# Optimization experiments

Hardware: AMD Instinct MI355X
Metric: run time of the kernel (lower is better)

## Reference

```python
import jax, jax.numpy as jnp
import numpy as np

N_HEADS = 16
HIDDEN = 1024
HEAD = HIDDEN // N_HEADS


def setup_inputs() -> dict:
    key = jax.random.key(0)
    ks = jax.random.split(key, 11)
    B, S, H = 2, 2048, HIDDEN
    s = 1.0 / np.sqrt(H)
    return {
        "query": jax.random.normal(ks[0], (B, S, H), jnp.float32),
        "key": jax.random.normal(ks[1], (B, S, H), jnp.float32),
        "value": jax.random.normal(ks[2], (B, S, H), jnp.float32),
        "Wq": jax.random.normal(ks[3], (H, H), jnp.float32) * s,
        "bq": jnp.zeros((H,), jnp.float32),
        "Wk": jax.random.normal(ks[4], (H, H), jnp.float32) * s,
        "bk": jnp.zeros((H,), jnp.float32),
        "Wv": jax.random.normal(ks[5], (H, H), jnp.float32) * s,
        "bv": jnp.zeros((H,), jnp.float32),
        "Wo": jax.random.normal(ks[6], (H, H), jnp.float32) * s,
        "bo": jnp.zeros((H,), jnp.float32),
    }


def reference(query, key, value, Wq, bq, Wk, bk, Wv, bv, Wo, bo):
    B, Sq, H = query.shape
    Sk = key.shape[1]
    # QKV projections, split heads: [B, n_heads, S, head]
    q = (query @ Wq + bq).reshape(B, Sq, N_HEADS, HEAD).transpose(0, 2, 1, 3)
    k = (key @ Wk + bk).reshape(B, Sk, N_HEADS, HEAD).transpose(0, 2, 1, 3)
    v = (value @ Wv + bv).reshape(B, Sk, N_HEADS, HEAD).transpose(0, 2, 1, 3)
    # scaled dot-product attention (no mask, dropout p=0)
    scores = jnp.einsum("bhqd,bhkd->bhqk", q, k) / np.sqrt(HEAD).astype(np.float32)
    attn = jax.nn.softmax(scores, axis=-1)
    out = jnp.einsum("bhqk,bhkd->bhqd", attn, v)
    out = out.transpose(0, 2, 1, 3).reshape(B, Sq, H)
    return out @ Wo + bo
```

## Files before the change

kernel.cpp:

```cpp
#include <hip/hip_runtime.h>
#include <hip/hip_bf16.h>
#include <stdint.h>

typedef unsigned short u16;
typedef short bf16x8 __attribute__((ext_vector_type(8)));
typedef float f32x4 __attribute__((ext_vector_type(4)));

#define DEVI static __device__ __forceinline__

#if __has_builtin(__builtin_amdgcn_exp2f)
#define EXP2F(x) __builtin_amdgcn_exp2f(x)
#else
#define EXP2F(x) exp2f(x)
#endif

DEVI u16 f2bf(float f) {
  union { float f; uint32_t u; } v; v.f = f;
  uint32_t u = v.u;
  u += 0x7fffu + ((u >> 16) & 1u);
  return (u16)(u >> 16);
}
DEVI uint32_t pk2bf(float lo, float hi) {
  __hip_bfloat162 h = __float22bfloat162_rn(float2{lo, hi});
  union { __hip_bfloat162 h; uint32_t u; } v; v.h = h; return v.u;
}

DEVI void async16(const void* g, const void* l) {
  __builtin_amdgcn_global_load_lds(
      (const __attribute__((address_space(1))) void*)g,
      (__attribute__((address_space(3))) void*)l, 16, 0, 0);
}

DEVI f32x4 mfma16(bf16x8 a, bf16x8 b, f32x4 c) {
  return __builtin_amdgcn_mfma_f32_16x16x32_bf16(a, b, c, 0, 0, 0);
}

#define CSC 0.18033688011112042f

__global__ void convx(const float* __restrict__ q, const float* __restrict__ k,
                      const float* __restrict__ v, u16* __restrict__ out) {
  const int z = blockIdx.y;
  const float* src = (z == 0) ? q : (z == 1) ? k : v;
  const int i = (blockIdx.x * 256 + threadIdx.x) * 4;
  float4 f = *(const float4*)(src + i);
  ushort4 o;
  o.x = f2bf(f.x); o.y = f2bf(f.y); o.z = f2bf(f.z); o.w = f2bf(f.w);
  *(ushort4*)(out + (size_t)z * 4194304 + i) = o;
}

__global__ void transw(const float* __restrict__ Wq, const float* __restrict__ Wk,
                       const float* __restrict__ Wv, const float* __restrict__ Wo,
                       u16* __restrict__ WT) {
  __shared__ u16 tile[64 * 68];
  const int z = blockIdx.z;
  const float* W = (z == 0) ? Wq : (z == 1) ? Wk : (z == 2) ? Wv : Wo;
  u16* out = WT + (size_t)z * 1048576;
  const int R0 = blockIdx.y * 64, C0 = blockIdx.x * 64;
  const int t = threadIdx.x;
#pragma unroll
  for (int it = 0; it < 16; ++it) {
    int j = it * 256 + t;
    int r = j >> 6, c = j & 63;
    tile[r * 68 + c] = f2bf(W[(size_t)(R0 + r) * 1024 + C0 + c]);
  }
  __syncthreads();
#pragma unroll
  for (int it = 0; it < 16; ++it) {
    int j = it * 256 + t;
    int c = j >> 6, r = j & 63;
    out[(size_t)(C0 + c) * 1024 + R0 + r] = tile[r * 68 + c];
  }
}

__global__ __launch_bounds__(256, 3)
void qkv_gemm(const u16* __restrict__ XB, const u16* __restrict__ WT,
              const float* __restrict__ bq, const float* __restrict__ bk,
              const float* __restrict__ bv,
              u16* __restrict__ QN, u16* __restrict__ KN, u16* __restrict__ VT) {
  __shared__ u16 smem[16896];
  u16* lA = smem;
  u16* lB = smem + 8192;
  const int z = blockIdx.y;
  const u16* A  = XB + (size_t)z * 4194304;
  const u16* Bt = WT + (size_t)z * 1048576;
  const float* bias = (z == 0) ? bq : (z == 1) ? bk : bv;
  const int T = blockIdx.x;
  const int m0 = (T & 31) * 128, n0 = (T >> 5) * 128;
  const int t = threadIdx.x, lane = t & 63, w = t >> 6;
  const int quad = lane >> 4, l16 = lane & 15;
  const int wm = (w & 1) * 64, wn = (w >> 1) * 64;

  f32x4 acc[4][4] = {};
  for (int kt = 0; kt < 16; ++kt) {
    const int k0 = kt * 64;
#pragma unroll
    for (int it = 0; it < 4; ++it) {
      int i = it * 256 + t;
      int r = i >> 3, cc = i & 7, c = cc ^ (r & 7);
      async16(A + (size_t)(m0 + r) * 1024 + k0 + c * 8, &lA[i * 8]);
      async16(Bt + (size_t)(n0 + r) * 1024 + k0 + c * 8, &lB[i * 8]);
    }
    __syncthreads();
#pragma unroll
    for (int ks = 0; ks < 2; ++ks) {
      bf16x8 af[4], bfr[4];
#pragma unroll
      for (int rt = 0; rt < 4; ++rt) {
        int row = wm + rt * 16 + l16;
        af[rt] = *(const bf16x8*)&lA[row * 64 + ((ks * 4 + quad) ^ (row & 7)) * 8];
      }
#pragma unroll
      for (int ct = 0; ct < 4; ++ct) {
        int row = wn + ct * 16 + l16;
        bfr[ct] = *(const bf16x8*)&lB[row * 64 + ((ks * 4 + quad) ^ (row & 7)) * 8];
      }
#pragma unroll
      for (int rt = 0; rt < 4; ++rt)
#pragma unroll
        for (int ct = 0; ct < 4; ++ct)
          acc[rt][ct] = mfma16(bfr[ct], af[rt], acc[rt][ct]);
    }
    __syncthreads();
  }

  if (z < 2) {
    const float scl = (z == 0) ? CSC : 1.0f;
#pragma unroll
    for (int rt = 0; rt < 4; ++rt) {
      int sl = wm + rt * 16 + l16;
#pragma unroll
      for (int ct = 0; ct < 4; ++ct) {
        int nb = wn + ct * 16 + quad * 4;
        float4 b4 = *(const float4*)&bias[n0 + nb];
        ushort4 pk;
        pk.x = f2bf((acc[rt][ct][0] + b4.x) * scl);
        pk.y = f2bf((acc[rt][ct][1] + b4.y) * scl);
        pk.z = f2bf((acc[rt][ct][2] + b4.z) * scl);
        pk.w = f2bf((acc[rt][ct][3] + b4.w) * scl);
        *(ushort4*)&smem[sl * 132 + nb] = pk;
      }
    }
    __syncthreads();
    u16* out = (z == 0) ? QN : KN;
#pragma unroll
    for (int p = 0; p < 8; ++p) {
      int idx = p * 256 + t;
      int row = idx >> 4, chunk = idx & 15;
      *(bf16x8*)&out[(size_t)(m0 + row) * 1024 + n0 + chunk * 8] =
          *(const bf16x8*)&smem[row * 132 + chunk * 8];
    }
  } else {
#pragma unroll
    for (int rt = 0; rt < 4; ++rt) {
      int sl = wm + rt * 16 + l16;
#pragma unroll
      for (int ct = 0; ct < 4; ++ct) {
        int nb = wn + ct * 16 + quad * 4;
        float4 b4 = *(const float4*)&bias[n0 + nb];
        smem[(nb + 0) * 132 + sl] = f2bf(acc[rt][ct][0] + b4.x);
        smem[(nb + 1) * 132 + sl] = f2bf(acc[rt][ct][1] + b4.y);
        smem[(nb + 2) * 132 + sl] = f2bf(acc[rt][ct][2] + b4.z);
        smem[(nb + 3) * 132 + sl] = f2bf(acc[rt][ct][3] + b4.w);
      }
    }
    __syncthreads();
    const int bb = m0 >> 11, sb = m0 & 2047;
#pragma unroll
    for (int p = 0; p < 8; ++p) {
      int idx = p * 256 + t;
      int dl = idx >> 4, chunk = idx & 15;
      int ncol = n0 + dl, hh = ncol >> 6, dd = ncol & 63;
      *(bf16x8*)&VT[((size_t)((bb * 16 + hh) * 64 + dd)) * 2048 + sb + chunk * 8] =
          *(const bf16x8*)&smem[dl * 132 + chunk * 8];
    }
  }
}

__global__ __launch_bounds__(512, 2)
void attn6(const u16* __restrict__ QN, const u16* __restrict__ KN,
           const u16* __restrict__ VT, u16* __restrict__ AO) {
  __shared__ u16 lK[2][64 * 64];
  __shared__ u16 lV[2][64 * 64];
  __shared__ u16 lPT[8][32 * 72];
  const int qt0 = blockIdx.x, h = blockIdx.y, b = blockIdx.z;
  const int t = threadIdx.x, lane = t & 63, w = t >> 6;
  const int quad = lane >> 4, l16 = lane & 15;
  const u16* Qg = QN + ((size_t)(b * 2048 + qt0 * 256)) * 1024 + h * 64;
  const u16* Kg = KN + ((size_t)b * 2048) * 1024 + h * 64;
  const u16* Vg = VT + ((size_t)((b * 16 + h) * 64)) * 2048;

  bf16x8 qf[2][2];
#pragma unroll
  for (int qs = 0; qs < 2; ++qs)
#pragma unroll
    for (int ks = 0; ks < 2; ++ks)
      qf[qs][ks] = *(const bf16x8*)(Qg + (size_t)(w * 32 + qs * 16 + l16) * 1024 +
                                    ks * 32 + quad * 8);

  {
    int r = t >> 3, cc = t & 7, c = cc ^ (r & 7);
    async16(Kg + (size_t)r * 1024 + c * 8, &lK[0][t * 8]);
    async16(Vg + (size_t)r * 2048 + c * 8, &lV[0][t * 8]);
  }
  __syncthreads();

  f32x4 o[2][4] = {};
  float lsum[2] = {0.f, 0.f};
  u16* myP = &lPT[w][0];

  for (int kt = 0; kt < 32; ++kt) {
    const int cur = kt & 1, nxt = cur ^ 1;
    if (kt + 1 < 32) {
      const int kb = (kt + 1) * 64;
      int r = t >> 3, cc = t & 7, c = cc ^ (r & 7);
      async16(Kg + (size_t)(kb + r) * 1024 + c * 8, &lK[nxt][t * 8]);
      async16(Vg + (size_t)r * 2048 + kb + c * 8, &lV[nxt][t * 8]);
    }

    f32x4 sc[2][4];
    __builtin_amdgcn_s_setprio(1);
#pragma unroll
    for (int st = 0; st < 4; ++st) {
      int row = st * 16 + l16;
      bf16x8 kf0 = *(const bf16x8*)&lK[cur][row * 64 + ((quad) ^ (row & 7)) * 8];
      bf16x8 kf1 = *(const bf16x8*)&lK[cur][row * 64 + ((4 + quad) ^ (row & 7)) * 8];
#pragma unroll
      for (int qs = 0; qs < 2; ++qs) {
        f32x4 z = {};
        sc[qs][st] = mfma16(kf0, qf[qs][0], z);
        sc[qs][st] = mfma16(kf1, qf[qs][1], sc[qs][st]);
      }
    }
    __builtin_amdgcn_s_setprio(0);

#pragma unroll
    for (int qs = 0; qs < 2; ++qs)
#pragma unroll
      for (int st = 0; st < 4; ++st) {
        float p0 = EXP2F(sc[qs][st][0]);
        float p1 = EXP2F(sc[qs][st][1]);
        float p2 = EXP2F(sc[qs][st][2]);
        float p3 = EXP2F(sc[qs][st][3]);
        lsum[qs] += (p0 + p1) + (p2 + p3);
        uint2 pk;
        pk.x = pk2bf(p0, p1);
        pk.y = pk2bf(p2, p3);
        *(uint2*)&myP[(qs * 16 + l16) * 72 + st * 16 + quad * 4] = pk;
      }

    __builtin_amdgcn_s_setprio(1);
#pragma unroll
    for (int ks2 = 0; ks2 < 2; ++ks2) {
      bf16x8 pf0 = *(const bf16x8*)&myP[(l16) * 72 + ks2 * 32 + quad * 8];
      bf16x8 pf1 = *(const bf16x8*)&myP[(16 + l16) * 72 + ks2 * 32 + quad * 8];
#pragma unroll
      for (int dt = 0; dt < 4; ++dt) {
        int row = dt * 16 + l16;
        bf16x8 vf = *(const bf16x8*)&lV[cur][row * 64 + ((ks2 * 4 + quad) ^ (row & 7)) * 8];
        o[0][dt] = mfma16(vf, pf0, o[0][dt]);
        o[1][dt] = mfma16(vf, pf1, o[1][dt]);
      }
    }
    __builtin_amdgcn_s_setprio(0);
    __syncthreads();
  }

#pragma unroll
  for (int qs = 0; qs < 2; ++qs) {
    float l = lsum[qs];
    l += __shfl_xor(l, 16, 64);
    l += __shfl_xor(l, 32, 64);
    float inv = 1.0f / l;
    int qglob = qt0 * 256 + w * 32 + qs * 16 + l16;
    size_t base = ((size_t)(b * 2048 + qglob)) * 1024 + h * 64;
#pragma unroll
    for (int dt = 0; dt < 4; ++dt) {
      ushort4 pk;
      pk.x = f2bf(o[qs][dt][0] * inv);
      pk.y = f2bf(o[qs][dt][1] * inv);
      pk.z = f2bf(o[qs][dt][2] * inv);
      pk.w = f2bf(o[qs][dt][3] * inv);
      *(ushort4*)&AO[base + dt * 16 + quad * 4] = pk;
    }
  }
}

__global__ __launch_bounds__(256, 2)
void oproj_gemm(const u16* __restrict__ AO, const u16* __restrict__ Bt,
                const float* __restrict__ bias, float* __restrict__ out) {
  __shared__ u16 lA[128 * 64];
  __shared__ u16 lB[64 * 64];
  const int T = blockIdx.x;
  const int m0 = (T & 31) * 128, n0 = (T >> 5) * 64;
  const int t = threadIdx.x, lane = t & 63, w = t >> 6;
  const int quad = lane >> 4, l16 = lane & 15;
  const int wm = (w & 1) * 64, wn = (w >> 1) * 32;

  f32x4 acc[4][2] = {};
  for (int kt = 0; kt < 16; ++kt) {
    const int k0 = kt * 64;
#pragma unroll
    for (int it = 0; it < 4; ++it) {
      int i = it * 256 + t;
      int r = i >> 3, cc = i & 7, c = cc ^ (r & 7);
      async16(AO + (size_t)(m0 + r) * 1024 + k0 + c * 8, &lA[i * 8]);
    }
#pragma unroll
    for (int it = 0; it < 2; ++it) {
      int i = it * 256 + t;
      int r = i >> 3, cc = i & 7, c = cc ^ (r & 7);
      async16(Bt + (size_t)(n0 + r) * 1024 + k0 + c * 8, &lB[i * 8]);
    }
    __syncthreads();
#pragma unroll
    for (int ks = 0; ks < 2; ++ks) {
      bf16x8 af[4], bfr[2];
#pragma unroll
      for (int rt = 0; rt < 4; ++rt) {
        int row = wm + rt * 16 + l16;
        af[rt] = *(const bf16x8*)&lA[row * 64 + ((ks * 4 + quad) ^ (row & 7)) * 8];
      }
#pragma unroll
      for (int ct = 0; ct < 2; ++ct) {
        int row = wn + ct * 16 + l16;
        bfr[ct] = *(const bf16x8*)&lB[row * 64 + ((ks * 4 + quad) ^ (row & 7)) * 8];
      }
#pragma unroll
      for (int rt = 0; rt < 4; ++rt)
#pragma unroll
        for (int ct = 0; ct < 2; ++ct)
          acc[rt][ct] = mfma16(af[rt], bfr[ct], acc[rt][ct]);
    }
    __syncthreads();
  }

#pragma unroll
  for (int ct = 0; ct < 2; ++ct) {
    int ncol = n0 + wn + ct * 16 + l16;
    float bvv = bias[ncol];
#pragma unroll
    for (int rt = 0; rt < 4; ++rt)
#pragma unroll
      for (int r = 0; r < 4; ++r) {
        int m = m0 + wm + rt * 16 + quad * 4 + r;
        out[(size_t)m * 1024 + ncol] = acc[rt][ct][r] + bvv;
      }
  }
}

extern "C" void kernel_launch(void* const* d_in, const int* in_sizes, int n_in,
                              void* d_out, int out_size, void* d_ws, size_t ws_size,
                              hipStream_t stream) {
  const float* query = (const float*)d_in[0];
  const float* key   = (const float*)d_in[1];
  const float* value = (const float*)d_in[2];
  const float* Wq = (const float*)d_in[3];
  const float* bq = (const float*)d_in[4];
  const float* Wk = (const float*)d_in[5];
  const float* bk = (const float*)d_in[6];
  const float* Wv = (const float*)d_in[7];
  const float* bv = (const float*)d_in[8];
  const float* Wo = (const float*)d_in[9];
  const float* bo = (const float*)d_in[10];
  float* out = (float*)d_out;

  u16* WT = (u16*)d_ws;
  u16* QN = WT + 4 * 1048576;
  u16* KN = QN + 4194304;
  u16* VT = KN + 4194304;
  u16* XB = VT + 4194304;
  u16* AO = XB;

  convx<<<dim3(4096, 3), 256, 0, stream>>>(query, key, value, XB);
  transw<<<dim3(16, 16, 4), 256, 0, stream>>>(Wq, Wk, Wv, Wo, WT);
  qkv_gemm<<<dim3(256, 3), 256, 0, stream>>>(XB, WT, bq, bk, bv, QN, KN, VT);
  attn6<<<dim3(8, 16, 2), 512, 0, stream>>>(QN, KN, VT, AO);
  oproj_gemm<<<dim3(512), 256, 0, stream>>>(AO, WT + 3 * 1048576, bo, out);
}
```

Before: 218.1 us.

## Halve attention block to 128 queries with 4 waves, double grid size

The attention kernel now uses 256-thread blocks covering 128 query rows instead of 512 threads covering 256. This doubles the grid to 512 blocks so the GPU's compute units fill more evenly, with a launch bound of 3 blocks per CU. Each thread now issues two async K/V tile loads. The P staging stride changes from 72 to 76, which alters the LDS bank pattern. The trade-off is that K/V tiles are reloaded twice as often across the grid, and the sync granularity per block changes.

Result: slower. 241.6 us (+10.8%).

```diff
diff --git a/kernel.cpp b/kernel.cpp
--- a/kernel.cpp
+++ b/kernel.cpp
@@ -36,6 +36,8 @@
 }
 
 #define CSC 0.18033688011112042f
+
+#define PSTR 76
 
 __global__ void convx(const float* __restrict__ q, const float* __restrict__ k,
                       const float* __restrict__ v, u16* __restrict__ out) {
@@ -176,16 +178,16 @@
   }
 }
 
-__global__ __launch_bounds__(512, 2)
-void attn6(const u16* __restrict__ QN, const u16* __restrict__ KN,
+__global__ __launch_bounds__(256, 3)
+void attn7(const u16* __restrict__ QN, const u16* __restrict__ KN,
            const u16* __restrict__ VT, u16* __restrict__ AO) {
   __shared__ u16 lK[2][64 * 64];
   __shared__ u16 lV[2][64 * 64];
-  __shared__ u16 lPT[8][32 * 72];
+  __shared__ u16 lPT[4][32 * PSTR];
   const int qt0 = blockIdx.x, h = blockIdx.y, b = blockIdx.z;
   const int t = threadIdx.x, lane = t & 63, w = t >> 6;
   const int quad = lane >> 4, l16 = lane & 15;
-  const u16* Qg = QN + ((size_t)(b * 2048 + qt0 * 256)) * 1024 + h * 64;
+  const u16* Qg = QN + ((size_t)(b * 2048 + qt0 * 128)) * 1024 + h * 64;
   const u16* Kg = KN + ((size_t)b * 2048) * 1024 + h * 64;
   const u16* Vg = VT + ((size_t)((b * 16 + h) * 64)) * 2048;
 
@@ -197,10 +199,12 @@
       qf[qs][ks] = *(const bf16x8*)(Qg + (size_t)(w * 32 + qs * 16 + l16) * 1024 +
                                     ks * 32 + quad * 8);
 
-  {
-    int r = t >> 3, cc = t & 7, c = cc ^ (r & 7);
-    async16(Kg + (size_t)r * 1024 + c * 8, &lK[0][t * 8]);
-    async16(Vg + (size_t)r * 2048 + c * 8, &lV[0][t * 8]);
+#pragma unroll
+  for (int p = 0; p < 2; ++p) {
+    int i = p * 256 + t;
+    int r = i >> 3, cc = i & 7, c = cc ^ (r & 7);
+    async16(Kg + (size_t)r * 1024 + c * 8, &lK[0][i * 8]);
+    async16(Vg + (size_t)r * 2048 + c * 8, &lV[0][i * 8]);
   }
   __syncthreads();
 
@@ -212,9 +216,13 @@
     const int cur = kt & 1, nxt = cur ^ 1;
     if (kt + 1 < 32) {
       const int kb = (kt + 1) * 64;
-      int r = t >> 3, cc = t & 7, c = cc ^ (r & 7);
-      async16(Kg + (size_t)(kb + r) * 1024 + c * 8, &lK[nxt][t * 8]);
-      async16(Vg + (size_t)r * 2048 + kb + c * 8, &lV[nxt][t * 8]);
+#pragma unroll
+      for (int p = 0; p < 2; ++p) {
+        int i = p * 256 + t;
+        int r = i >> 3, cc = i & 7, c = cc ^ (r & 7);
+        async16(Kg + (size_t)(kb + r) * 1024 + c * 8, &lK[nxt][i * 8]);
+        async16(Vg + (size_t)r * 2048 + kb + c * 8, &lV[nxt][i * 8]);
+      }
     }
 
     f32x4 sc[2][4];
@@ -245,14 +253,14 @@
         uint2 pk;
         pk.x = pk2bf(p0, p1);
         pk.y = pk2bf(p2, p3);
-        *(uint2*)&myP[(qs * 16 + l16) * 72 + st * 16 + quad * 4] = pk;
+        *(uint2*)&myP[(qs * 16 + l16) * PSTR + st * 16 + quad * 4] = pk;
       }
 
     __builtin_amdgcn_s_setprio(1);
 #pragma unroll
     for (int ks2 = 0; ks2 < 2; ++ks2) {
-      bf16x8 pf0 = *(const bf16x8*)&myP[(l16) * 72 + ks2 * 32 + quad * 8];
-      bf16x8 pf1 = *(const bf16x8*)&myP[(16 + l16) * 72 + ks2 * 32 + quad * 8];
+      bf16x8 pf0 = *(const bf16x8*)&myP[(l16) * PSTR + ks2 * 32 + quad * 8];
+      bf16x8 pf1 = *(const bf16x8*)&myP[(16 + l16) * PSTR + ks2 * 32 + quad * 8];
 #pragma unroll
       for (int dt = 0; dt < 4; ++dt) {
         int row = dt * 16 + l16;
@@ -271,7 +279,7 @@
     l += __shfl_xor(l, 16, 64);
     l += __shfl_xor(l, 32, 64);
     float inv = 1.0f / l;
-    int qglob = qt0 * 256 + w * 32 + qs * 16 + l16;
+    int qglob = qt0 * 128 + w * 32 + qs * 16 + l16;
     size_t base = ((size_t)(b * 2048 + qglob)) * 1024 + h * 64;
 #pragma unroll
     for (int dt = 0; dt < 4; ++dt) {
@@ -374,6 +382,6 @@
   convx<<<dim3(4096, 3), 256, 0, stream>>>(query, key, value, XB);
   transw<<<dim3(16, 16, 4), 256, 0, stream>>>(Wq, Wk, Wv, Wo, WT);
   qkv_gemm<<<dim3(256, 3), 256, 0, stream>>>(XB, WT, bq, bk, bv, QN, KN, VT);
-  attn6<<<dim3(8, 16, 2), 512, 0, stream>>>(QN, KN, VT, AO);
+  attn7<<<dim3(16, 16, 2), 256, 0, stream>>>(QN, KN, VT, AO);
   oproj_gemm<<<dim3(512), 256, 0, stream>>>(AO, WT + 3 * 1048576, bo, out);
 }
```
